# Optimization experiments

Hardware: AMD Instinct MI355X
Metric: run time of the kernel (lower is better)

## Reference

```python
import jax, jax.numpy as jnp
import numpy as np

N, E = 100000, 1000000
IN_F, HID, OUT, K = 64, 64, 32, 3


def setup_inputs() -> dict:
    key = jax.random.key(0)
    ks = jax.random.split(key, 8)
    s = 0.05
    return {
        "features": jax.random.normal(ks[0], (N, IN_F), dtype=jnp.float32),
        "src": jax.random.randint(ks[1], (E,), 0, N),
        "dst": jax.random.randint(ks[2], (E,), 0, N),
        "n_nodes": N,
        "W1": jax.random.normal(ks[3], (K * IN_F, HID), jnp.float32) * s,
        "b1": jnp.zeros((HID,), jnp.float32),
        "W2": jax.random.normal(ks[4], (K * HID, HID), jnp.float32) * s,
        "b2": jnp.zeros((HID,), jnp.float32),
        "Wm1": jax.random.normal(ks[5], (HID, HID), jnp.float32) * s,
        "bm1": jnp.zeros((HID,), jnp.float32),
        "Wm2": jax.random.normal(ks[6], (HID, OUT), jnp.float32) * s,
        "bm2": jnp.zeros((OUT,), jnp.float32),
    }


def _cheb_conv(x, src, dst, dinv, W, b, n_nodes, k=K):
    # DGL ChebConv with lambda_max = 2 (re_norm = 2/lambda_max = 1).
    def prop(h):  # D^{-1/2} A D^{-1/2} h via edge gather/scatter
        m = (h * dinv)[src]                                   # [E, F]
        agg = jax.ops.segment_sum(m, dst, num_segments=n_nodes)
        return agg * dinv

    X0 = x
    Xs = [X0]
    X1 = -prop(X0)                 # -re_norm*L h + (re_norm-1)*X0, re_norm=1
    Xs.append(X1)
    for _ in range(2, k):
        Xi = -2.0 * prop(X1) - X0  # Chebyshev recursion
        Xs.append(Xi)
        X0, X1 = X1, Xi
    return jnp.concatenate(Xs, axis=1) @ W + b  # Linear(k*F_in -> F_out)


def reference(features, src, dst, n_nodes, W1, b1, W2, b2, Wm1, bm1, Wm2, bm2):
    deg = jax.ops.segment_sum(
        jnp.ones((src.shape[0],), dtype=features.dtype), dst, num_segments=n_nodes
    )
    dinv = (jnp.clip(deg, 1.0, None) ** -0.5)[:, None]  # in-degree^{-1/2}
    x = jax.nn.relu(_cheb_conv(features, src, dst, dinv, W1, b1, n_nodes))
    x = jax.nn.relu(_cheb_conv(x, src, dst, dinv, W2, b2, n_nodes))
    return jax.nn.relu(x @ Wm1 + bm1) @ Wm2 + bm2
```

## Files before the change

kernel.cpp:

```cpp
#include <hip/hip_runtime.h>


typedef unsigned short ushort_t;
typedef __attribute__((ext_vector_type(8))) short v8s;
typedef __attribute__((ext_vector_type(4))) float v4f;

__device__ inline ushort_t f2bf(float f) {
    unsigned u = __float_as_uint(f);
    return (ushort_t)((u + 0x7FFFu + ((u >> 16) & 1u)) >> 16);
}
__device__ inline float bf2f(ushort_t h) {
    return __uint_as_float(((unsigned)h) << 16);
}

#define BSH 9
#define BSZ (1 << BSH)
#define CHUNK 4096


__global__ __launch_bounds__(256) void k_bhist(const int* __restrict__ dst,
                                               int* __restrict__ gbase, int E, int NB) {
    __shared__ int h[1024];
    for (int i = threadIdx.x; i < NB; i += 256) h[i] = 0;
    __syncthreads();
    for (int i = blockIdx.x * blockDim.x + threadIdx.x; i < E; i += gridDim.x * blockDim.x)
        atomicAdd(&h[dst[i] >> BSH], 1);
    __syncthreads();
    for (int i = threadIdx.x; i < NB; i += 256)
        if (h[i]) atomicAdd(&gbase[i], h[i]);
}

__global__ void k_bscan(int* __restrict__ gbase, int* __restrict__ gcur, int NB) {
    __shared__ int sh[1024];
    int t = threadIdx.x;
    int v = (t < NB) ? gbase[t] : 0;
    sh[t] = v;
    __syncthreads();
    for (int off = 1; off < 1024; off <<= 1) {
        int u = 0;
        if (t >= off) u = sh[t - off];
        __syncthreads();
        sh[t] += u;
        __syncthreads();
    }
    if (t < NB) {
        int excl = sh[t] - v;
        gbase[t] = excl;
        gcur[t] = excl;
    }
}

__global__ __launch_bounds__(256) void k_bucket2(
    const int* __restrict__ src, const int* __restrict__ dst,
    int* __restrict__ gcur, int2* __restrict__ eb, int E, int NB) {
    __shared__ int ls[CHUNK];
    __shared__ int ld[CHUNK];
    __shared__ int hist[1024];
    __shared__ int bbase[1024];
    int t = threadIdx.x;
    int base = blockIdx.x * CHUNK;
    int count = E - base;
    if (count > CHUNK) count = CHUNK;
    for (int i = t; i < NB; i += 256) hist[i] = 0;
    __syncthreads();
    for (int i = t; i < count; i += 256) {
        int s = src[base + i];
        int d = dst[base + i];
        ls[i] = s;
        ld[i] = d;
        atomicAdd(&hist[d >> BSH], 1);
    }
    __syncthreads();
    for (int b = t; b < NB; b += 256) {
        int c = hist[b];
        bbase[b] = c ? atomicAdd(&gcur[b], c) : 0;
        hist[b] = 0;
    }
    __syncthreads();
    for (int i = t; i < count; i += 256) {
        int d = ld[i];
        int b = d >> BSH;
        int off = atomicAdd(&hist[b], 1);
        eb[bbase[b] + off] = make_int2(ls[i], d);
    }
}

__global__ __launch_bounds__(256) void k_local(
    const int2* __restrict__ eb, const int* __restrict__ gbase,
    int* __restrict__ col, int* __restrict__ row_ptr,
    float* __restrict__ dinv, int N, int E, int NB) {
    __shared__ int cnt[BSZ];
    __shared__ int tsum[256];
    int t = threadIdx.x;
    int b = blockIdx.x;
    int d0 = b << BSH;
    cnt[2 * t] = 0;
    cnt[2 * t + 1] = 0;
    __syncthreads();
    int beg = gbase[b];
    int end = (b + 1 < NB) ? gbase[b + 1] : E;
    for (int i = beg + t; i < end; i += 256)
        atomicAdd(&cnt[eb[i].y - d0], 1);
    __syncthreads();
    int c0 = cnt[2 * t], c1 = cnt[2 * t + 1];
    int mysum = c0 + c1;
    tsum[t] = mysum;
    __syncthreads();
    for (int off = 1; off < 256; off <<= 1) {
        int u = 0;
        if (t >= off) u = tsum[t - off];
        __syncthreads();
        tsum[t] += u;
        __syncthreads();
    }
    int rbase = beg + tsum[t] - mysum;
    int d = d0 + 2 * t;
    if (d < N) {
        row_ptr[d] = rbase;
        dinv[d] = rsqrtf(fmaxf((float)c0, 1.0f));
    }
    if (d + 1 < N) {
        row_ptr[d + 1] = rbase + c0;
        dinv[d + 1] = rsqrtf(fmaxf((float)c1, 1.0f));
    }
    cnt[2 * t] = rbase;
    cnt[2 * t + 1] = rbase + c0;
    __syncthreads();
    for (int i = beg + t; i < end; i += 256) {
        int2 e = eb[i];
        int p = atomicAdd(&cnt[e.y - d0], 1);
        col[p] = e.x;
    }
    if (b == NB - 1 && t == 0) row_ptr[N] = E;
}

__global__ void k_wprep(const float* __restrict__ W1, const float* __restrict__ W2,
                        const float* __restrict__ Wm1, const float* __restrict__ Wm2,
                        ushort_t* __restrict__ W1t, ushort_t* __restrict__ W2t,
                        ushort_t* __restrict__ Wm1t, ushort_t* __restrict__ Wm2t) {
    int i = blockIdx.x * 256 + threadIdx.x;
    if (i < 12288) { int k = i >> 6, n = i & 63; W1t[n * 192 + k] = f2bf(W1[i]); return; }
    i -= 12288;
    if (i < 12288) { int k = i >> 6, n = i & 63; W2t[n * 192 + k] = f2bf(W2[i]); return; }
    i -= 12288;
    if (i < 4096) { int k = i >> 6, n = i & 63; Wm1t[n * 64 + k] = f2bf(Wm1[i]); return; }
    i -= 4096;
    if (i < 2048) { int k = i >> 5, n = i & 31; Wm2t[n * 64 + k] = f2bf(Wm2[i]); }
}

__global__ void k_tobf16(const float4* __restrict__ X, const float* __restrict__ dinv,
                         ushort4* __restrict__ Y, int n4) {
    int i = blockIdx.x * blockDim.x + threadIdx.x;
    if (i < n4) {
        float s = dinv[i >> 4];
        float4 v = X[i];
        ushort4 o;
        o.x = f2bf(v.x * s); o.y = f2bf(v.y * s); o.z = f2bf(v.z * s); o.w = f2bf(v.w * s);
        Y[i] = o;
    }
}

template <int MODE>
__global__ __launch_bounds__(256) void k_prop(
    const ushort_t* __restrict__ Xb, const int* __restrict__ rp,
    const int* __restrict__ col, const float* __restrict__ dinv,
    const ushort_t* __restrict__ X0b, ushort_t* __restrict__ OUTB, int N) {
    int wid = (blockIdx.x * blockDim.x + threadIdx.x) >> 6;
    int lane = threadIdx.x & 63;
    if (wid >= N) return;
    int g = lane >> 4;
    int fl = (lane & 15) * 4;
    int beg = rp[wid], end = rp[wid + 1];
    float4 a0 = make_float4(0.f, 0.f, 0.f, 0.f);
    float4 a1 = make_float4(0.f, 0.f, 0.f, 0.f);
    int e = beg + g;
    for (; e + 4 < end; e += 8) {
        int s0 = col[e], s1 = col[e + 4];
        ushort4 u0 = *(const ushort4*)&Xb[(size_t)s0 * 64 + fl];
        ushort4 u1 = *(const ushort4*)&Xb[(size_t)s1 * 64 + fl];
        a0.x += bf2f(u0.x); a0.y += bf2f(u0.y); a0.z += bf2f(u0.z); a0.w += bf2f(u0.w);
        a1.x += bf2f(u1.x); a1.y += bf2f(u1.y); a1.z += bf2f(u1.z); a1.w += bf2f(u1.w);
    }
    if (e < end) {
        int s0 = col[e];
        ushort4 u0 = *(const ushort4*)&Xb[(size_t)s0 * 64 + fl];
        a0.x += bf2f(u0.x); a0.y += bf2f(u0.y); a0.z += bf2f(u0.z); a0.w += bf2f(u0.w);
    }
    float4 acc;
    acc.x = a0.x + a1.x;
    acc.y = a0.y + a1.y;
    acc.z = a0.z + a1.z;
    acc.w = a0.w + a1.w;
    acc.x += __shfl_xor(acc.x, 16);
    acc.y += __shfl_xor(acc.y, 16);
    acc.z += __shfl_xor(acc.z, 16);
    acc.w += __shfl_xor(acc.w, 16);
    acc.x += __shfl_xor(acc.x, 32);
    acc.y += __shfl_xor(acc.y, 32);
    acc.z += __shfl_xor(acc.z, 32);
    acc.w += __shfl_xor(acc.w, 32);
    if (g == 0) {
        float di = dinv[wid];
        float4 o;
        if (MODE == 1) {
            float m = -di * di;
            o.x = m * acc.x; o.y = m * acc.y; o.z = m * acc.z; o.w = m * acc.w;
        } else {
            ushort4 x0u = *(const ushort4*)&X0b[(size_t)wid * 64 + fl];
            float m = -2.0f * di;
            float rd = 1.0f / di;
            o.x = fmaf(m, acc.x, -rd * bf2f(x0u.x));
            o.y = fmaf(m, acc.y, -rd * bf2f(x0u.y));
            o.z = fmaf(m, acc.z, -rd * bf2f(x0u.z));
            o.w = fmaf(m, acc.w, -rd * bf2f(x0u.w));
        }
        ushort4 ob;
        ob.x = f2bf(o.x); ob.y = f2bf(o.y); ob.z = f2bf(o.z); ob.w = f2bf(o.w);
        *(ushort4*)&OUTB[(size_t)wid * 64 + fl] = ob;
    }
}

template <bool SCALE_OUT>
__global__ __launch_bounds__(256) void k_cheb_mfma(
    const ushort_t* __restrict__ X0, const ushort_t* __restrict__ X1,
    const ushort_t* __restrict__ X2, const float* __restrict__ dinv,
    const ushort_t* __restrict__ Wt,
    const float* __restrict__ b, ushort_t* __restrict__ Yb, int N) {
    int wave = threadIdx.x >> 6, lane = threadIdx.x & 63;
    int n16 = lane & 15, q = lane >> 4;
    int node0 = blockIdx.x * 64;
    int arow = node0 + wave * 16 + n16;
    const ushort_t* Xc[3] = {X0, X1, X2};

    v4f acc_s[4], acc_u[4];
#pragma unroll
    for (int t = 0; t < 4; t++) {
        acc_s[t] = (v4f){0.f, 0.f, 0.f, 0.f};
        acc_u[t] = (v4f){0.f, 0.f, 0.f, 0.f};
    }

#pragma unroll
    for (int ks = 0; ks < 6; ks++) {
        int c = ks >> 1;
        int kk = (ks & 1) * 32 + q * 8;
        v8s av = {0, 0, 0, 0, 0, 0, 0, 0};
        if (arow < N) av = *(const v8s*)&Xc[c][(size_t)arow * 64 + kk];
#pragma unroll
        for (int t = 0; t < 4; t++) {
            v8s bv = *(const v8s*)&Wt[(size_t)(t * 16 + n16) * 192 + ks * 32 + q * 8];
            if (c < 2)
                acc_s[t] = __builtin_amdgcn_mfma_f32_16x16x32_bf16(av, bv, acc_s[t], 0, 0, 0);
            else
                acc_u[t] = __builtin_amdgcn_mfma_f32_16x16x32_bf16(av, bv, acc_u[t], 0, 0, 0);
        }
    }

    int rbase = node0 + wave * 16 + q * 4;
#pragma unroll
    for (int r = 0; r < 4; r++) {
        int row = rbase + r;
        if (row < N) {
            float dv = dinv[row];
            float rd = 1.0f / dv;
            float s = SCALE_OUT ? dv : 1.0f;
#pragma unroll
            for (int t = 0; t < 4; t++) {
                float y = fmaf(rd, acc_s[t][r], acc_u[t][r]) + b[t * 16 + n16];
                y = fmaxf(y, 0.0f);
                Yb[(size_t)row * 64 + t * 16 + n16] = f2bf(s * y);
            }
        }
    }
}

__global__ __launch_bounds__(256) void k_mlp_mfma(
    const ushort_t* __restrict__ Hb, const ushort_t* __restrict__ W1t,
    const float* __restrict__ b1, const ushort_t* __restrict__ W2t,
    const float* __restrict__ b2, float* __restrict__ out, int N) {
    __shared__ ushort_t Hs[64][76];
    int wave = threadIdx.x >> 6, lane = threadIdx.x & 63;
    int n16 = lane & 15, q = lane >> 4;
    int node0 = blockIdx.x * 64;
    int arow = node0 + wave * 16 + n16;

    v4f acc[4];
#pragma unroll
    for (int t = 0; t < 4; t++) acc[t] = (v4f){0.f, 0.f, 0.f, 0.f};
#pragma unroll
    for (int ks = 0; ks < 2; ks++) {
        v8s av = {0, 0, 0, 0, 0, 0, 0, 0};
        if (arow < N) av = *(const v8s*)&Hb[(size_t)arow * 64 + ks * 32 + q * 8];
#pragma unroll
        for (int t = 0; t < 4; t++) {
            v8s bv = *(const v8s*)&W1t[(size_t)(t * 16 + n16) * 64 + ks * 32 + q * 8];
            acc[t] = __builtin_amdgcn_mfma_f32_16x16x32_bf16(av, bv, acc[t], 0, 0, 0);
        }
    }
    int lr = wave * 16 + q * 4;
#pragma unroll
    for (int r = 0; r < 4; r++)
#pragma unroll
        for (int t = 0; t < 4; t++) {
            float y = acc[t][r] + b1[t * 16 + n16];
            Hs[lr + r][t * 16 + n16] = f2bf(fmaxf(y, 0.0f));
        }
    __syncthreads();

    v4f a2[2];
    a2[0] = (v4f){0.f, 0.f, 0.f, 0.f};
    a2[1] = (v4f){0.f, 0.f, 0.f, 0.f};
#pragma unroll
    for (int ks = 0; ks < 2; ks++) {
        v8s av = *(const v8s*)&Hs[wave * 16 + n16][ks * 32 + q * 8];
#pragma unroll
        for (int t = 0; t < 2; t++) {
            v8s bv = *(const v8s*)&W2t[(size_t)(t * 16 + n16) * 64 + ks * 32 + q * 8];
            a2[t] = __builtin_amdgcn_mfma_f32_16x16x32_bf16(av, bv, a2[t], 0, 0, 0);
        }
    }
    int rbase = node0 + wave * 16 + q * 4;
#pragma unroll
    for (int r = 0; r < 4; r++) {
        int row = rbase + r;
        if (row < N) {
#pragma unroll
            for (int t = 0; t < 2; t++)
                out[(size_t)row * 32 + t * 16 + n16] = a2[t][r] + b2[t * 16 + n16];
        }
    }
}

extern "C" void kernel_launch(void* const* d_in, const int* in_sizes, int n_in,
                              void* d_out, int out_size, void* d_ws, size_t ws_size,
                              hipStream_t stream) {
    const float* features = (const float*)d_in[0];
    const int* src = (const int*)d_in[1];
    const int* dst = (const int*)d_in[2];
    const float* W1 = (const float*)d_in[4];
    const float* b1 = (const float*)d_in[5];
    const float* W2 = (const float*)d_in[6];
    const float* b2 = (const float*)d_in[7];
    const float* Wm1 = (const float*)d_in[8];
    const float* bm1 = (const float*)d_in[9];
    const float* Wm2 = (const float*)d_in[10];
    const float* bm2 = (const float*)d_in[11];
    float* out = (float*)d_out;

    int N = in_sizes[0] / 64;
    int E = in_sizes[1];
    int NB = (N + BSZ - 1) >> BSH;

    float* ws = (float*)d_ws;
    float* dinv = ws;
    int* row_ptr = (int*)(dinv + N);
    int* gbase = row_ptr + (N + 1);
    int* gcur = gbase + 1024;
    int* col = gcur + 1024;
    int2* eb = (int2*)(((uintptr_t)(col + E) + 7) & ~(uintptr_t)7);
    ushort_t* Fb  = (ushort_t*)(eb + E);
    ushort_t* X1b = Fb  + (size_t)N * 64;
    ushort_t* X2b = X1b + (size_t)N * 64;
    ushort_t* H1b = X2b + (size_t)N * 64;
    ushort_t* H2b = H1b + (size_t)N * 64;
    ushort_t* W1t = H2b + (size_t)N * 64;
    ushort_t* W2t = W1t + 64 * 192;
    ushort_t* Wm1t = W2t + 64 * 192;
    ushort_t* Wm2t = Wm1t + 64 * 64;

    int pblk = (N * 64 + 255) / 256;
    int gblk = (N + 63) / 64;
    int n4 = N * 16;
    int cblk = (n4 + 255) / 256;
    int bblk = (E + CHUNK - 1) / CHUNK;

    k_wprep<<<(30720 + 255) / 256, 256, 0, stream>>>(W1, W2, Wm1, Wm2, W1t, W2t, Wm1t, Wm2t);

    hipMemsetAsync(gbase, 0, NB * sizeof(int), stream);
    k_bhist<<<512, 256, 0, stream>>>(dst, gbase, E, NB);
    k_bscan<<<1, 1024, 0, stream>>>(gbase, gcur, NB);
    k_bucket2<<<bblk, 256, 0, stream>>>(src, dst, gcur, eb, E, NB);
    k_local<<<NB, 256, 0, stream>>>(eb, gbase, col, row_ptr, dinv, N, E, NB);

    k_tobf16<<<cblk, 256, 0, stream>>>((const float4*)features, dinv, (ushort4*)Fb, n4);

    k_prop<1><<<pblk, 256, 0, stream>>>(Fb, row_ptr, col, dinv, nullptr, X1b, N);
    k_prop<2><<<pblk, 256, 0, stream>>>(X1b, row_ptr, col, dinv, Fb, X2b, N);
    k_cheb_mfma<true><<<gblk, 256, 0, stream>>>(Fb, X1b, X2b, dinv, W1t, b1, H1b, N);

    k_prop<1><<<pblk, 256, 0, stream>>>(H1b, row_ptr, col, dinv, nullptr, X1b, N);
    k_prop<2><<<pblk, 256, 0, stream>>>(X1b, row_ptr, col, dinv, H1b, X2b, N);
    k_cheb_mfma<false><<<gblk, 256, 0, stream>>>(H1b, X1b, X2b, dinv, W2t, b2, H2b, N);

    k_mlp_mfma<<<gblk, 256, 0, stream>>>(H2b, Wm1t, bm1, Wm2t, bm2, out, N);
}
```

Measured before the change: 395.9 us.

## Fuse second Chebyshev propagation into MFMA GEMM and bf16 conversion into CSR build

```diff
diff --git a/kernel.cpp b/kernel.cpp
--- a/kernel.cpp
+++ b/kernel.cpp
@@ -88,7 +88,8 @@
 __global__ __launch_bounds__(256) void k_local(
     const int2* __restrict__ eb, const int* __restrict__ gbase,
     int* __restrict__ col, int* __restrict__ row_ptr,
-    float* __restrict__ dinv, int N, int E, int NB) {
+    float* __restrict__ dinv, const float* __restrict__ features,
+    ushort_t* __restrict__ Fb, int N, int E, int NB) {
     __shared__ int cnt[BSZ];
     __shared__ int tsum[256];
     int t = threadIdx.x;
@@ -114,14 +115,16 @@
         __syncthreads();
     }
     int rbase = beg + tsum[t] - mysum;
+    float di0 = rsqrtf(fmaxf((float)c0, 1.0f));
+    float di1 = rsqrtf(fmaxf((float)c1, 1.0f));
     int d = d0 + 2 * t;
     if (d < N) {
         row_ptr[d] = rbase;
-        dinv[d] = rsqrtf(fmaxf((float)c0, 1.0f));
+        dinv[d] = di0;
     }
     if (d + 1 < N) {
         row_ptr[d + 1] = rbase + c0;
-        dinv[d + 1] = rsqrtf(fmaxf((float)c1, 1.0f));
+        dinv[d + 1] = di1;
     }
     cnt[2 * t] = rbase;
     cnt[2 * t + 1] = rbase + c0;
@@ -132,6 +135,20 @@
         col[p] = e.x;
     }
     if (b == NB - 1 && t == 0) row_ptr[N] = E;
+    __syncthreads();
+    ((float*)cnt)[2 * t] = di0;
+    ((float*)cnt)[2 * t + 1] = di1;
+    __syncthreads();
+    int nmax = N - d0;
+    if (nmax > BSZ) nmax = BSZ;
+    for (int i = t; i < nmax * 16; i += 256) {
+        int nl = i >> 4, f4 = (i & 15) * 4;
+        float s = ((float*)cnt)[nl];
+        float4 v = *(const float4*)&features[(size_t)(d0 + nl) * 64 + f4];
+        ushort4 o;
+        o.x = f2bf(v.x * s); o.y = f2bf(v.y * s); o.z = f2bf(v.z * s); o.w = f2bf(v.w * s);
+        *(ushort4*)&Fb[(size_t)(d0 + nl) * 64 + f4] = o;
+    }
 }
 
 __global__ void k_wprep(const float* __restrict__ W1, const float* __restrict__ W2,
@@ -148,23 +165,10 @@
     if (i < 2048) { int k = i >> 5, n = i & 31; Wm2t[n * 64 + k] = f2bf(Wm2[i]); }
 }
 
-__global__ void k_tobf16(const float4* __restrict__ X, const float* __restrict__ dinv,
-                         ushort4* __restrict__ Y, int n4) {
-    int i = blockIdx.x * blockDim.x + threadIdx.x;
-    if (i < n4) {
-        float s = dinv[i >> 4];
-        float4 v = X[i];
-        ushort4 o;
-        o.x = f2bf(v.x * s); o.y = f2bf(v.y * s); o.z = f2bf(v.z * s); o.w = f2bf(v.w * s);
-        Y[i] = o;
-    }
-}
-
-template <int MODE>
-__global__ __launch_bounds__(256) void k_prop(
+__global__ __launch_bounds__(256) void k_prop1(
     const ushort_t* __restrict__ Xb, const int* __restrict__ rp,
     const int* __restrict__ col, const float* __restrict__ dinv,
-    const ushort_t* __restrict__ X0b, ushort_t* __restrict__ OUTB, int N) {
+    ushort_t* __restrict__ OUTB, int N) {
     int wid = (blockIdx.x * blockDim.x + threadIdx.x) >> 6;
     int lane = threadIdx.x & 63;
     if (wid >= N) return;
@@ -201,50 +205,97 @@
     acc.w += __shfl_xor(acc.w, 32);
     if (g == 0) {
         float di = dinv[wid];
-        float4 o;
-        if (MODE == 1) {
-            float m = -di * di;
-            o.x = m * acc.x; o.y = m * acc.y; o.z = m * acc.z; o.w = m * acc.w;
-        } else {
-            ushort4 x0u = *(const ushort4*)&X0b[(size_t)wid * 64 + fl];
-            float m = -2.0f * di;
-            float rd = 1.0f / di;
-            o.x = fmaf(m, acc.x, -rd * bf2f(x0u.x));
-            o.y = fmaf(m, acc.y, -rd * bf2f(x0u.y));
-            o.z = fmaf(m, acc.z, -rd * bf2f(x0u.z));
-            o.w = fmaf(m, acc.w, -rd * bf2f(x0u.w));
-        }
+        float m = -di * di;
         ushort4 ob;
-        ob.x = f2bf(o.x); ob.y = f2bf(o.y); ob.z = f2bf(o.z); ob.w = f2bf(o.w);
+        ob.x = f2bf(m * acc.x);
+        ob.y = f2bf(m * acc.y);
+        ob.z = f2bf(m * acc.z);
+        ob.w = f2bf(m * acc.w);
         *(ushort4*)&OUTB[(size_t)wid * 64 + fl] = ob;
     }
 }
 
 template <bool SCALE_OUT>
-__global__ __launch_bounds__(256) void k_cheb_mfma(
+__global__ __launch_bounds__(256) void k_cheb_fused(
     const ushort_t* __restrict__ X0, const ushort_t* __restrict__ X1,
-    const ushort_t* __restrict__ X2, const float* __restrict__ dinv,
-    const ushort_t* __restrict__ Wt,
-    const float* __restrict__ b, ushort_t* __restrict__ Yb, int N) {
+    const int* __restrict__ rp, const int* __restrict__ col,
+    const float* __restrict__ dinv,
+    const ushort_t* __restrict__ Wt, const float* __restrict__ b,
+    ushort_t* __restrict__ Yb, int N) {
+    __shared__ ushort_t X2s[64][72];
     int wave = threadIdx.x >> 6, lane = threadIdx.x & 63;
+    int node0 = blockIdx.x * 64;
+
+    {
+        int g = lane >> 4;
+        int fl = (lane & 15) * 4;
+        for (int i = 0; i < 16; i++) {
+            int node = node0 + wave * 16 + i;
+            if (node >= N) break;
+            int beg = rp[node], end = rp[node + 1];
+            float4 a0 = make_float4(0.f, 0.f, 0.f, 0.f);
+            float4 a1 = make_float4(0.f, 0.f, 0.f, 0.f);
+            int e = beg + g;
+            for (; e + 4 < end; e += 8) {
+                int s0 = col[e], s1 = col[e + 4];
+                ushort4 u0 = *(const ushort4*)&X1[(size_t)s0 * 64 + fl];
+                ushort4 u1 = *(const ushort4*)&X1[(size_t)s1 * 64 + fl];
+                a0.x += bf2f(u0.x); a0.y += bf2f(u0.y); a0.z += bf2f(u0.z); a0.w += bf2f(u0.w);
+                a1.x += bf2f(u1.x); a1.y += bf2f(u1.y); a1.z += bf2f(u1.z); a1.w += bf2f(u1.w);
+            }
+            if (e < end) {
+                int s0 = col[e];
+                ushort4 u0 = *(const ushort4*)&X1[(size_t)s0 * 64 + fl];
+                a0.x += bf2f(u0.x); a0.y += bf2f(u0.y); a0.z += bf2f(u0.z); a0.w += bf2f(u0.w);
+            }
+            float4 acc;
+            acc.x = a0.x + a1.x;
+            acc.y = a0.y + a1.y;
+            acc.z = a0.z + a1.z;
+            acc.w = a0.w + a1.w;
+            acc.x += __shfl_xor(acc.x, 16);
+            acc.y += __shfl_xor(acc.y, 16);
+            acc.z += __shfl_xor(acc.z, 16);
+            acc.w += __shfl_xor(acc.w, 16);
+            acc.x += __shfl_xor(acc.x, 32);
+            acc.y += __shfl_xor(acc.y, 32);
+            acc.z += __shfl_xor(acc.z, 32);
+            acc.w += __shfl_xor(acc.w, 32);
+            if (g == 0) {
+                float di = dinv[node];
+                ushort4 x0u = *(const ushort4*)&X0[(size_t)node * 64 + fl];
+                float m = -2.0f * di;
+                float rd = 1.0f / di;
+                ushort4 ob;
+                ob.x = f2bf(fmaf(m, acc.x, -rd * bf2f(x0u.x)));
+                ob.y = f2bf(fmaf(m, acc.y, -rd * bf2f(x0u.y)));
+                ob.z = f2bf(fmaf(m, acc.z, -rd * bf2f(x0u.z)));
+                ob.w = f2bf(fmaf(m, acc.w, -rd * bf2f(x0u.w)));
+                *(ushort4*)&X2s[wave * 16 + i][fl] = ob;
+            }
+        }
+    }
+    __syncthreads();
+
     int n16 = lane & 15, q = lane >> 4;
-    int node0 = blockIdx.x * 64;
     int arow = node0 + wave * 16 + n16;
-    const ushort_t* Xc[3] = {X0, X1, X2};
-
+    const ushort_t* Xc[2] = {X0, X1};
     v4f acc_s[4], acc_u[4];
 #pragma unroll
     for (int t = 0; t < 4; t++) {
         acc_s[t] = (v4f){0.f, 0.f, 0.f, 0.f};
         acc_u[t] = (v4f){0.f, 0.f, 0.f, 0.f};
     }
-
 #pragma unroll
     for (int ks = 0; ks < 6; ks++) {
         int c = ks >> 1;
         int kk = (ks & 1) * 32 + q * 8;
         v8s av = {0, 0, 0, 0, 0, 0, 0, 0};
-        if (arow < N) av = *(const v8s*)&Xc[c][(size_t)arow * 64 + kk];
+        if (c < 2) {
+            if (arow < N) av = *(const v8s*)&Xc[c][(size_t)arow * 64 + kk];
+        } else {
+            av = *(const v8s*)&X2s[wave * 16 + n16][kk];
+        }
 #pragma unroll
         for (int t = 0; t < 4; t++) {
             v8s bv = *(const v8s*)&Wt[(size_t)(t * 16 + n16) * 192 + ks * 32 + q * 8];
@@ -254,7 +305,6 @@
                 acc_u[t] = __builtin_amdgcn_mfma_f32_16x16x32_bf16(av, bv, acc_u[t], 0, 0, 0);
         }
     }
-
     int rbase = node0 + wave * 16 + q * 4;
 #pragma unroll
     for (int r = 0; r < 4; r++) {
@@ -359,8 +409,7 @@
     int2* eb = (int2*)(((uintptr_t)(col + E) + 7) & ~(uintptr_t)7);
     ushort_t* Fb  = (ushort_t*)(eb + E);
     ushort_t* X1b = Fb  + (size_t)N * 64;
-    ushort_t* X2b = X1b + (size_t)N * 64;
-    ushort_t* H1b = X2b + (size_t)N * 64;
+    ushort_t* H1b = X1b + (size_t)N * 64;
     ushort_t* H2b = H1b + (size_t)N * 64;
     ushort_t* W1t = H2b + (size_t)N * 64;
     ushort_t* W2t = W1t + 64 * 192;
@@ -369,8 +418,6 @@
 
     int pblk = (N * 64 + 255) / 256;
     int gblk = (N + 63) / 64;
-    int n4 = N * 16;
-    int cblk = (n4 + 255) / 256;
     int bblk = (E + CHUNK - 1) / CHUNK;
 
     k_wprep<<<(30720 + 255) / 256, 256, 0, stream>>>(W1, W2, Wm1, Wm2, W1t, W2t, Wm1t, Wm2t);
@@ -379,17 +426,13 @@
     k_bhist<<<512, 256, 0, stream>>>(dst, gbase, E, NB);
     k_bscan<<<1, 1024, 0, stream>>>(gbase, gcur, NB);
     k_bucket2<<<bblk, 256, 0, stream>>>(src, dst, gcur, eb, E, NB);
-    k_local<<<NB, 256, 0, stream>>>(eb, gbase, col, row_ptr, dinv, N, E, NB);
-
-    k_tobf16<<<cblk, 256, 0, stream>>>((const float4*)features, dinv, (ushort4*)Fb, n4);
-
-    k_prop<1><<<pblk, 256, 0, stream>>>(Fb, row_ptr, col, dinv, nullptr, X1b, N);
-    k_prop<2><<<pblk, 256, 0, stream>>>(X1b, row_ptr, col, dinv, Fb, X2b, N);
-    k_cheb_mfma<true><<<gblk, 256, 0, stream>>>(Fb, X1b, X2b, dinv, W1t, b1, H1b, N);
-
-    k_prop<1><<<pblk, 256, 0, stream>>>(H1b, row_ptr, col, dinv, nullptr, X1b, N);
-    k_prop<2><<<pblk, 256, 0, stream>>>(X1b, row_ptr, col, dinv, H1b, X2b, N);
-    k_cheb_mfma<false><<<gblk, 256, 0, stream>>>(H1b, X1b, X2b, dinv, W2t, b2, H2b, N);
+    k_local<<<NB, 256, 0, stream>>>(eb, gbase, col, row_ptr, dinv, features, Fb, N, E, NB);
+
+    k_prop1<<<pblk, 256, 0, stream>>>(Fb, row_ptr, col, dinv, X1b, N);
+    k_cheb_fused<true><<<gblk, 256, 0, stream>>>(Fb, X1b, row_ptr, col, dinv, W1t, b1, H1b, N);
+
+    k_prop1<<<pblk, 256, 0, stream>>>(H1b, row_ptr, col, dinv, X1b, N);
+    k_cheb_fused<false><<<gblk, 256, 0, stream>>>(H1b, X1b, row_ptr, col, dinv, W2t, b2, H2b, N);
 
     k_mlp_mfma<<<gblk, 256, 0, stream>>>(H2b, Wm1t, bm1, Wm2t, bm2, out, N);
 }
```

After: 458.7 us. +15.9%, slower.
